# Kernel optimization log

Hardware: AMD Instinct MI355X
Metric: run time of the kernel (lower is better)

The kernel has to match this reference:

```python
import jax, jax.numpy as jnp
import numpy as np

LN_EPS = 1e-5


def setup_inputs() -> dict:
    key = jax.random.key(0)
    ks = jax.random.split(key, 8)
    B, C, H, W = 16, 768, 64, 64
    cond_dim = 1024
    inp = {}
    inp["spatial_features"] = jax.random.normal(ks[0], (B, C, H, W), dtype=jnp.float32)
    inp["conditioning"] = jax.random.normal(ks[1], (B, cond_dim), dtype=jnp.float32)
    # conditioning_proj: Linear(cond_dim -> C)
    inp["w_cond"] = jax.random.normal(ks[2], (C, cond_dim), dtype=jnp.float32) * 0.02
    inp["b_cond"] = jnp.zeros((C,), dtype=jnp.float32)
    # MultiheadAttention packed in-projection [3C, C] and bias [3C]
    inp["in_proj_w"] = jax.random.normal(ks[3], (3 * C, C), dtype=jnp.float32) * 0.02
    inp["in_proj_b"] = jnp.zeros((3 * C,), dtype=jnp.float32)
    # MHA out_proj
    inp["attn_out_w"] = jax.random.normal(ks[4], (C, C), dtype=jnp.float32) * 0.02
    inp["attn_out_b"] = jnp.zeros((C,), dtype=jnp.float32)
    # output_proj Linear (dropout is identity at inference)
    inp["w_out"] = jax.random.normal(ks[5], (C, C), dtype=jnp.float32) * 0.02
    inp["b_out"] = jnp.zeros((C,), dtype=jnp.float32)
    # LayerNorm affine
    inp["ln_gamma"] = jnp.ones((C,), dtype=jnp.float32)
    inp["ln_beta"] = jnp.zeros((C,), dtype=jnp.float32)
    return inp


def reference(spatial_features, conditioning, w_cond, b_cond, in_proj_w, in_proj_b,
              attn_out_w, attn_out_b, w_out, b_out, ln_gamma, ln_beta):
    B, C, H, W = spatial_features.shape
    S = H * W
    # [B, C, H, W] -> [B, S, C]
    spatial_flat = spatial_features.reshape(B, C, S).transpose(0, 2, 1)
    # conditioning projection -> single KV token per batch: [B, C]
    cond = conditioning @ w_cond.T + b_cond
    # With a single key, softmax over the key axis is identically 1, so the
    # attention output is exactly the value vector broadcast over all queries;
    # Q and K projections have zero effect on output (and zero gradient).
    wv = in_proj_w[2 * C:]          # value rows of packed in-projection
    bv = in_proj_b[2 * C:]
    v = cond @ wv.T + bv            # [B, C]
    attn = v @ attn_out_w.T + attn_out_b  # MHA out_proj, [B, C]
    # output_proj (dropout = identity in eval)
    proj = attn @ w_out.T + b_out   # [B, C]
    # residual + LayerNorm over channel dim
    x = spatial_flat + proj[:, None, :]  # [B, S, C]
    mu = jnp.mean(x, axis=-1, keepdims=True)
    var = jnp.mean(jnp.square(x - mu), axis=-1, keepdims=True)
    y = (x - mu) * jax.lax.rsqrt(var + LN_EPS) * ln_gamma + ln_beta
    # [B, S, C] -> [B, C, H, W]
    return y.transpose(0, 2, 1).reshape(B, C, H, W)
```

## Files before the change

kernel.cpp:

```cpp
#include <hip/hip_runtime.h>

#define CDIM 768
#define SDIM 4096
#define SV (SDIM / 4)

__global__ __launch_bounds__(256) void small_gemm_kernel(
    const float* __restrict__ X, const float* __restrict__ W,
    const float* __restrict__ bias, float* __restrict__ out,
    int Cn, int K)
{
    int gid  = blockIdx.x * blockDim.x + threadIdx.x;
    int wid  = gid >> 6;
    int lane = threadIdx.x & 63;
    int total = 16 * Cn;
    if (wid >= total) return;
    int b = wid / Cn;
    int c = wid - b * Cn;
    const float* x = X + (size_t)b * K;
    const float* w = W + (size_t)c * K;
    float acc = 0.f;
    for (int k = lane * 4; k < K; k += 256) {
        float4 xv = *(const float4*)(x + k);
        float4 wv = *(const float4*)(w + k);
        acc += xv.x * wv.x + xv.y * wv.y + xv.z * wv.z + xv.w * wv.w;
    }
#pragma unroll
    for (int m = 32; m; m >>= 1) acc += __shfl_xor(acc, m, 64);
    if (lane == 0) out[wid] = acc + bias[c];
}

__global__ __launch_bounds__(64) void fused_add_ln_kernel(
    const float* __restrict__ sp, const float* __restrict__ proj,
    const float* __restrict__ gamma, const float* __restrict__ beta,
    float* __restrict__ out)
{
    __shared__ float s_proj[CDIM], s_gamma[CDIM], s_beta[CDIM];
    const int b    = blockIdx.y;
    const int s0   = blockIdx.x * 64;
    const int lane = threadIdx.x;
    for (int i = lane; i < CDIM; i += 64) {
        s_proj[i]  = proj[b * CDIM + i];
        s_gamma[i] = gamma[i];
        s_beta[i]  = beta[i];
    }
    __syncthreads();

    const int si = lane & 15;
    const int cg = lane >> 4;
    const int c0 = cg * (CDIM / 4);
    const int c1 = c0 + (CDIM / 4);

    const float4* spv  = (const float4*)(sp  + (size_t)b * CDIM * SDIM + s0);
    float4*       outv = (float4*)      (out + (size_t)b * CDIM * SDIM + s0);

    float sx = 0, sy = 0, sz = 0, sw = 0;
    float qx = 0, qy = 0, qz = 0, qw = 0;
    for (int c = c0; c < c1; ++c) {
        float4 t = spv[(size_t)c * SV + si];
        float  p = s_proj[c];
        t.x += p; t.y += p; t.z += p; t.w += p;
        sx += t.x; sy += t.y; sz += t.z; sw += t.w;
        qx += t.x * t.x; qy += t.y * t.y; qz += t.z * t.z; qw += t.w * t.w;
    }
#pragma unroll
    for (int m = 16; m <= 32; m <<= 1) {
        sx += __shfl_xor(sx, m, 64); sy += __shfl_xor(sy, m, 64);
        sz += __shfl_xor(sz, m, 64); sw += __shfl_xor(sw, m, 64);
        qx += __shfl_xor(qx, m, 64); qy += __shfl_xor(qy, m, 64);
        qz += __shfl_xor(qz, m, 64); qw += __shfl_xor(qw, m, 64);
    }
    const float inv = 1.f / CDIM;
    const float mux = sx * inv, muy = sy * inv, muz = sz * inv, muw = sw * inv;
    const float rx = rsqrtf(qx * inv - mux * mux + 1e-5f);
    const float ry = rsqrtf(qy * inv - muy * muy + 1e-5f);
    const float rz = rsqrtf(qz * inv - muz * muz + 1e-5f);
    const float rw = rsqrtf(qw * inv - muw * muw + 1e-5f);

    for (int c = c0; c < c1; ++c) {
        float4 t = spv[(size_t)c * SV + si];
        float  p  = s_proj[c];
        float  g  = s_gamma[c];
        float  be = s_beta[c];
        float4 y;
        y.x = (t.x + p - mux) * rx * g + be;
        y.y = (t.y + p - muy) * ry * g + be;
        y.z = (t.z + p - muz) * rz * g + be;
        y.w = (t.w + p - muw) * rw * g + be;
        outv[(size_t)c * SV + si] = y;
    }
}

extern "C" void kernel_launch(void* const* d_in, const int* in_sizes, int n_in,
                              void* d_out, int out_size, void* d_ws, size_t ws_size,
                              hipStream_t stream) {
    const float* sp           = (const float*)d_in[0];
    const float* conditioning = (const float*)d_in[1];
    const float* w_cond       = (const float*)d_in[2];
    const float* b_cond       = (const float*)d_in[3];
    const float* in_proj_w    = (const float*)d_in[4];
    const float* in_proj_b    = (const float*)d_in[5];
    const float* attn_out_w   = (const float*)d_in[6];
    const float* attn_out_b   = (const float*)d_in[7];
    const float* w_out        = (const float*)d_in[8];
    const float* b_out        = (const float*)d_in[9];
    const float* ln_gamma     = (const float*)d_in[10];
    const float* ln_beta      = (const float*)d_in[11];
    float* out = (float*)d_out;
    float* ws  = (float*)d_ws;

    float* cond = ws;
    float* v    = ws + 12288;
    float* attn = ws + 24576;
    float* proj = ws + 36864;

    const int gemm_blocks = (16 * CDIM * 64) / 256;
    small_gemm_kernel<<<gemm_blocks, 256, 0, stream>>>(
        conditioning, w_cond, b_cond, cond, CDIM, 1024);
    small_gemm_kernel<<<gemm_blocks, 256, 0, stream>>>(
        cond, in_proj_w + 2 * CDIM * CDIM, in_proj_b + 2 * CDIM, v, CDIM, CDIM);
    small_gemm_kernel<<<gemm_blocks, 256, 0, stream>>>(
        v, attn_out_w, attn_out_b, attn, CDIM, CDIM);
    small_gemm_kernel<<<gemm_blocks, 256, 0, stream>>>(
        attn, w_out, b_out, proj, CDIM, CDIM);

    dim3 grid(SDIM / 64, 16);
    fused_add_ln_kernel<<<grid, 64, 0, stream>>>(sp, proj, ln_gamma, ln_beta, out);
}
```

Measured before the change: 431.7 us.

## Widen LayerNorm blocks to 256 threads with shared-memory reduction and nontemporal stores

The add+LayerNorm kernel now runs 256 threads per block instead of 64. Each block still covers 64 spatial positions, but 16 channel groups each handle 48 channels, so partial sums and sums of squares are reduced through shared memory instead of wave shuffles. The loops are unrolled by 4, and output writes use nontemporal stores to avoid polluting the cache. This raises parallelism per block and memory-level parallelism, at the cost of two extra block barriers and a small serial reduction done by 16 threads.

```diff
diff --git a/kernel.cpp b/kernel.cpp
--- a/kernel.cpp
+++ b/kernel.cpp
@@ -3,6 +3,8 @@
 #define CDIM 768
 #define SDIM 4096
 #define SV (SDIM / 4)
+
+typedef float nfloat4 __attribute__((ext_vector_type(4)));
 
 __global__ __launch_bounds__(256) void small_gemm_kernel(
     const float* __restrict__ X, const float* __restrict__ W,
@@ -29,64 +31,83 @@
     if (lane == 0) out[wid] = acc + bias[c];
 }
 
-__global__ __launch_bounds__(64) void fused_add_ln_kernel(
+__global__ __launch_bounds__(256) void fused_add_ln_kernel(
     const float* __restrict__ sp, const float* __restrict__ proj,
     const float* __restrict__ gamma, const float* __restrict__ beta,
     float* __restrict__ out)
 {
     __shared__ float s_proj[CDIM], s_gamma[CDIM], s_beta[CDIM];
-    const int b    = blockIdx.y;
-    const int s0   = blockIdx.x * 64;
-    const int lane = threadIdx.x;
-    for (int i = lane; i < CDIM; i += 64) {
+    __shared__ float4 red_s[16][16];
+    __shared__ float4 red_q[16][16];
+    __shared__ float4 s_mu[16];
+    __shared__ float4 s_rs[16];
+
+    const int b  = blockIdx.y;
+    const int s0 = blockIdx.x * 64;
+    const int t  = threadIdx.x;
+    for (int i = t; i < CDIM; i += 256) {
         s_proj[i]  = proj[b * CDIM + i];
         s_gamma[i] = gamma[i];
         s_beta[i]  = beta[i];
     }
     __syncthreads();
 
-    const int si = lane & 15;
-    const int cg = lane >> 4;
-    const int c0 = cg * (CDIM / 4);
-    const int c1 = c0 + (CDIM / 4);
+    const int si = t & 15;
+    const int cg = t >> 4;
+    const int c0 = cg * (CDIM / 16);
+    const int c1 = c0 + (CDIM / 16);
 
     const float4* spv  = (const float4*)(sp  + (size_t)b * CDIM * SDIM + s0);
-    float4*       outv = (float4*)      (out + (size_t)b * CDIM * SDIM + s0);
+    nfloat4*      outv = (nfloat4*)     (out + (size_t)b * CDIM * SDIM + s0);
 
     float sx = 0, sy = 0, sz = 0, sw = 0;
     float qx = 0, qy = 0, qz = 0, qw = 0;
+#pragma unroll 4
     for (int c = c0; c < c1; ++c) {
-        float4 t = spv[(size_t)c * SV + si];
+        float4 v = spv[(size_t)c * SV + si];
         float  p = s_proj[c];
-        t.x += p; t.y += p; t.z += p; t.w += p;
-        sx += t.x; sy += t.y; sz += t.z; sw += t.w;
-        qx += t.x * t.x; qy += t.y * t.y; qz += t.z * t.z; qw += t.w * t.w;
+        v.x += p; v.y += p; v.z += p; v.w += p;
+        sx += v.x; sy += v.y; sz += v.z; sw += v.w;
+        qx += v.x * v.x; qy += v.y * v.y; qz += v.z * v.z; qw += v.w * v.w;
     }
+    red_s[cg][si] = make_float4(sx, sy, sz, sw);
+    red_q[cg][si] = make_float4(qx, qy, qz, qw);
+    __syncthreads();
+
+    if (t < 16) {
+        float4 S = make_float4(0, 0, 0, 0), Q = make_float4(0, 0, 0, 0);
 #pragma unroll
-    for (int m = 16; m <= 32; m <<= 1) {
-        sx += __shfl_xor(sx, m, 64); sy += __shfl_xor(sy, m, 64);
-        sz += __shfl_xor(sz, m, 64); sw += __shfl_xor(sw, m, 64);
-        qx += __shfl_xor(qx, m, 64); qy += __shfl_xor(qy, m, 64);
-        qz += __shfl_xor(qz, m, 64); qw += __shfl_xor(qw, m, 64);
+        for (int g = 0; g < 16; ++g) {
+            float4 a = red_s[g][t], q = red_q[g][t];
+            S.x += a.x; S.y += a.y; S.z += a.z; S.w += a.w;
+            Q.x += q.x; Q.y += q.y; Q.z += q.z; Q.w += q.w;
+        }
+        const float inv = 1.f / CDIM;
+        float4 mu = make_float4(S.x * inv, S.y * inv, S.z * inv, S.w * inv);
+        float4 rs;
+        rs.x = rsqrtf(Q.x * inv - mu.x * mu.x + 1e-5f);
+        rs.y = rsqrtf(Q.y * inv - mu.y * mu.y + 1e-5f);
+        rs.z = rsqrtf(Q.z * inv - mu.z * mu.z + 1e-5f);
+        rs.w = rsqrtf(Q.w * inv - mu.w * mu.w + 1e-5f);
+        s_mu[t] = mu;
+        s_rs[t] = rs;
     }
-    const float inv = 1.f / CDIM;
-    const float mux = sx * inv, muy = sy * inv, muz = sz * inv, muw = sw * inv;
-    const float rx = rsqrtf(qx * inv - mux * mux + 1e-5f);
-    const float ry = rsqrtf(qy * inv - muy * muy + 1e-5f);
-    const float rz = rsqrtf(qz * inv - muz * muz + 1e-5f);
-    const float rw = rsqrtf(qw * inv - muw * muw + 1e-5f);
+    __syncthreads();
 
+    const float4 mu = s_mu[si];
+    const float4 rs = s_rs[si];
+#pragma unroll 4
     for (int c = c0; c < c1; ++c) {
-        float4 t = spv[(size_t)c * SV + si];
+        float4 v = spv[(size_t)c * SV + si];
         float  p  = s_proj[c];
         float  g  = s_gamma[c];
         float  be = s_beta[c];
-        float4 y;
-        y.x = (t.x + p - mux) * rx * g + be;
-        y.y = (t.y + p - muy) * ry * g + be;
-        y.z = (t.z + p - muz) * rz * g + be;
-        y.w = (t.w + p - muw) * rw * g + be;
-        outv[(size_t)c * SV + si] = y;
+        nfloat4 y;
+        y.x = (v.x + p - mu.x) * rs.x * g + be;
+        y.y = (v.y + p - mu.y) * rs.y * g + be;
+        y.z = (v.z + p - mu.z) * rs.z * g + be;
+        y.w = (v.w + p - mu.w) * rs.w * g + be;
+        __builtin_nontemporal_store(y, &outv[(size_t)c * SV + si]);
     }
 }
 
@@ -124,5 +145,5 @@
         attn, w_out, b_out, proj, CDIM, CDIM);
 
     dim3 grid(SDIM / 64, 16);
-    fused_add_ln_kernel<<<grid, 64, 0, stream>>>(sp, proj, ln_gamma, ln_beta, out);
+    fused_add_ln_kernel<<<grid, 256, 0, stream>>>(sp, proj, ln_gamma, ln_beta, out);
 }
```

New measurement: 421.4 us. -2.4%, faster.
